# Optimization experiments

Measured on AMD Instinct MI355X. Metric: run time of the kernel, lower is better.

The kernel has to match this reference:

```python
import jax, jax.numpy as jnp
import numpy as np

B, L, H = 4, 1024, 1024
NH, HD = 16, 64
ND = NH * HD
ITERS = 4
U = 5  # MSA1 ring window size (hard-coded in source)


def _conv1x1(w, b, x):  # w [O,C], b [O], x [B,C,L] -> [B,O,L]  (Conv2d 1x1 == per-position linear)
    return jnp.einsum('oc,bcl->bol', w, x) + b[None, :, None]


def _layernorm(x, s, b, eps=1e-5):  # x [B,H,L]; LayerNorm over channel dim H
    mu = x.mean(1, keepdims=True)
    var = ((x - mu) ** 2).mean(1, keepdims=True)
    return (x - mu) / jnp.sqrt(var + eps) * s[None, :, None] + b[None, :, None]


def _msa1(x, ax, wq, bq, wk, bk, wv, bv, wo, bo):
    # x [B,H,L] normalized nodes; ax [B,H,2,L] (ring embedding + relay)
    b, h, l = x.shape
    q = _conv1x1(wq, bq, x).reshape(b, NH, HD, l)
    k = _conv1x1(wk, bk, x).reshape(b, NH, HD, l)
    v = _conv1x1(wv, bv, x).reshape(b, NH, HD, l)
    pad = U // 2
    kp = jnp.pad(k, ((0, 0), (0, 0), (0, 0), (pad, pad)))
    vp = jnp.pad(v, ((0, 0), (0, 0), (0, 0), (pad, pad)))
    # F.unfold with (U,1) kernel along L == stack of U shifted views
    kw = jnp.stack([kp[..., u:u + l] for u in range(U)], axis=3)  # [B,NH,HD,U,L]
    vw = jnp.stack([vp[..., u:u + l] for u in range(U)], axis=3)
    al = ax.shape[2]
    ak = (jnp.einsum('oc,bcal->boal', wk, ax) + bk[None, :, None, None]).reshape(b, NH, HD, al, l)
    av = (jnp.einsum('oc,bcal->boal', wv, ax) + bv[None, :, None, None]).reshape(b, NH, HD, al, l)
    kw = jnp.concatenate([kw, ak], axis=3)  # [B,NH,HD,U+2,L]
    vw = jnp.concatenate([vw, av], axis=3)
    scores = (q[:, :, :, None, :] * kw).sum(2) / np.sqrt(HD)  # [B,NH,U+2,L]
    alphas = jax.nn.softmax(scores, axis=2)
    att = (alphas[:, :, None, :, :] * vw).sum(3).reshape(b, ND, l)
    return _conv1x1(wo, bo, att)  # [B,H,L]


def _msa2(relay, y, smask, wq, bq, wk, bk, wo, bo):
    # relay [B,H]; y [B,H,L+1]; smask [B,L+1] True at padding
    b = relay.shape[0]
    q = (jnp.einsum('oc,bc->bo', wq, relay) + bq).reshape(b, NH, HD)
    k = _conv1x1(wk, bk, y).reshape(b, NH, HD, -1)
    pre = jnp.einsum('bnd,bndl->bnl', q, k) / np.sqrt(HD)
    pre = jnp.where(smask[:, None, :], -1e10, pre)
    alphas = jax.nn.softmax(pre, axis=-1)
    # NOTE: source has v = k (WV output unused) -- reproduced faithfully
    att = jnp.einsum('bnl,bndl->bnd', alphas, k).reshape(b, ND)
    return jnp.einsum('oc,bc->bo', wo, att) + bo  # [B,H]


def _star_forward(data, mask, ln_s, ln_b, rwq, rwq_b, rwk, rwk_b, rwv, rwv_b, rwo, rwo_b,
                  swq, swq_b, swk, swk_b, swo, swo_b):
    b, l, h = data.shape
    pad_mask = (mask == 0)  # True at padding positions
    smask = jnp.concatenate([jnp.zeros((b, 1), bool), pad_mask], axis=1)  # [B,L+1]
    embs = jnp.transpose(data, (0, 2, 1))  # [B,H,L]
    nodes = embs
    relay = embs.mean(2)  # [B,H]
    for i in range(ITERS):
        xn = _layernorm(nodes, ln_s[i], ln_b[i])
        ax = jnp.stack([embs, jnp.broadcast_to(relay[:, :, None], embs.shape)], axis=2)  # [B,H,2,L]
        ring = _msa1(xn, ax, rwq[i], rwq_b[i], rwk[i], rwk_b[i], rwv[i], rwv_b[i], rwo[i], rwo_b[i])
        nodes = nodes + jax.nn.leaky_relu(ring)
        y = jnp.concatenate([relay[:, :, None], nodes], axis=2)  # [B,H,L+1]
        relay = jax.nn.leaky_relu(_msa2(relay, y, smask, swq[i], swq_b[i], swk[i], swk_b[i], swo[i], swo_b[i]))
        nodes = jnp.where(pad_mask[:, None, :], 0.0, nodes)
    return jnp.transpose(nodes, (0, 2, 1)), relay  # [B,L,H], [B,H]


def setup_inputs() -> dict:
    key = jax.random.key(0)
    ks = jax.random.split(key, 16)
    def p(k, shape):
        return jax.random.normal(k, shape, jnp.float32) * 0.02
    return dict(
        data=jax.random.normal(ks[0], (B, L, H), jnp.float32),
        mask=jax.random.randint(ks[1], (B, L), 0, 2).astype(jnp.int32),
        ln_s=jnp.ones((ITERS, H), jnp.float32),
        ln_b=jnp.zeros((ITERS, H), jnp.float32),
        rwq=p(ks[2], (ITERS, ND, H)), rwq_b=p(ks[3], (ITERS, ND)),
        rwk=p(ks[4], (ITERS, ND, H)), rwk_b=p(ks[5], (ITERS, ND)),
        rwv=p(ks[6], (ITERS, ND, H)), rwv_b=p(ks[7], (ITERS, ND)),
        rwo=p(ks[8], (ITERS, H, ND)), rwo_b=p(ks[9], (ITERS, H)),
        swq=p(ks[10], (ITERS, ND, H)), swq_b=p(ks[11], (ITERS, ND)),
        swk=p(ks[12], (ITERS, ND, H)), swk_b=p(ks[13], (ITERS, ND)),
        swo=p(ks[14], (ITERS, H, ND)), swo_b=p(ks[15], (ITERS, H)),
    )


def reference(data, mask, ln_s, ln_b, rwq, rwq_b, rwk, rwk_b, rwv, rwv_b, rwo, rwo_b,
              swq, swq_b, swk, swk_b, swo, swo_b):
    return _star_forward(data, mask, ln_s, ln_b, rwq, rwq_b, rwk, rwk_b, rwv, rwv_b,
                         rwo, rwo_b, swq, swq_b, swk, swk_b, swo, swo_b)
```

## Files before the change

### kernel.cpp

```cpp
#include <hip/hip_runtime.h>
#include <math.h>

namespace {

constexpr int B_ = 4, L_ = 1024, H_ = 1024, NH_ = 16, HD_ = 64, ND_ = 1024, ITERS_ = 4;

typedef unsigned short u16;
typedef __attribute__((ext_vector_type(8))) short short8;
typedef __attribute__((ext_vector_type(4))) float f32x4;

__device__ inline u16 f2bf(float f) {
  unsigned u = __builtin_bit_cast(unsigned, f);
  u += 0x7FFFu + ((u >> 16) & 1u);
  return (u16)(u >> 16);
}
__device__ inline float bf2f(u16 v) {
  unsigned u = ((unsigned)v) << 16;
  return __builtin_bit_cast(float, u);
}

__device__ inline void gl_lds16(const u16* g, u16* l) {
  __builtin_amdgcn_global_load_lds((const __attribute__((address_space(1))) void*)g,
                                   (__attribute__((address_space(3))) void*)l, 16, 0, 0);
}

__global__ void k_prep(const float* __restrict__ data, const float* __restrict__ rwq,
                       const float* __restrict__ rwk, const float* __restrict__ rwv,
                       const float* __restrict__ rwo, const float* __restrict__ swk,
                       u16* __restrict__ embs_bf, u16* __restrict__ wq_bf,
                       u16* __restrict__ wk_bf, u16* __restrict__ wv_bf,
                       u16* __restrict__ wo_bf, u16* __restrict__ swk_bf,
                       float* __restrict__ nodes) {
  int i = blockIdx.x * 256 + threadIdx.x;
  int which = blockIdx.y;
  if (which == 6) {
    reinterpret_cast<float4*>(nodes)[i] = reinterpret_cast<const float4*>(data)[i];
    return;
  }
  const float* src;
  u16* dst;
  switch (which) {
    case 0: src = data; dst = embs_bf; break;
    case 1: src = rwq; dst = wq_bf; break;
    case 2: src = rwk; dst = wk_bf; break;
    case 3: src = rwv; dst = wv_bf; break;
    case 4: src = rwo; dst = wo_bf; break;
    default: src = swk; dst = swk_bf; break;
  }
  float4 v = reinterpret_cast<const float4*>(src)[i];
  ushort4 o;
  o.x = f2bf(v.x); o.y = f2bf(v.y); o.z = f2bf(v.z); o.w = f2bf(v.w);
  reinterpret_cast<ushort4*>(dst)[i] = o;
}

__global__ void k_relay_part(const float* __restrict__ data, float* __restrict__ part) {
  int b = blockIdx.z, chunk = blockIdx.y;
  int c = blockIdx.x * 256 + threadIdx.x;
  const float* p = data + ((size_t)b * L_ + chunk * 128) * H_ + c;
  float acc = 0.f;
  for (int l = 0; l < 128; ++l) acc += p[(size_t)l * H_];
  part[((size_t)b * 8 + chunk) * H_ + c] = acc;
}
__global__ void k_relay_reduce(const float* __restrict__ part, float* __restrict__ relay) {
  int i = blockIdx.x * 256 + threadIdx.x;
  int b = i >> 10, c = i & 1023;
  float acc = 0.f;
  for (int j = 0; j < 8; ++j) acc += part[((size_t)b * 8 + j) * H_ + c];
  relay[i] = acc * (1.f / (float)L_);
}

__global__ __launch_bounds__(256) void k_layernorm_bf(float* __restrict__ nodes,
                                                      const float* __restrict__ s,
                                                      const float* __restrict__ bb,
                                                      const int* __restrict__ mask,
                                                      u16* __restrict__ y, int do_zero) {
  int row = blockIdx.x * 4 + (threadIdx.x >> 6);
  int lane = threadIdx.x & 63;
  int b = row >> 10, l = row & 1023;
  bool pad = do_zero && (mask[b * L_ + l] == 0);
  float4* xr = reinterpret_cast<float4*>(nodes + (size_t)row * H_);
  float4 v[4];
  float sum = 0.f, sq = 0.f;
#pragma unroll
  for (int j = 0; j < 4; ++j) {
    v[j] = pad ? float4{0.f, 0.f, 0.f, 0.f} : xr[lane + 64 * j];
    sum += v[j].x + v[j].y + v[j].z + v[j].w;
    sq += v[j].x * v[j].x + v[j].y * v[j].y + v[j].z * v[j].z + v[j].w * v[j].w;
  }
  if (pad) {
#pragma unroll
    for (int j = 0; j < 4; ++j) xr[lane + 64 * j] = float4{0.f, 0.f, 0.f, 0.f};
  }
#pragma unroll
  for (int off = 32; off; off >>= 1) {
    sum += __shfl_xor(sum, off);
    sq += __shfl_xor(sq, off);
  }
  float mu = sum * (1.f / (float)H_);
  float rstd = rsqrtf(sq * (1.f / (float)H_) - mu * mu + 1e-5f);
  ushort4* yr = reinterpret_cast<ushort4*>(y + (size_t)row * H_);
#pragma unroll
  for (int j = 0; j < 4; ++j) {
    int c4 = lane + 64 * j;
    float4 sc = reinterpret_cast<const float4*>(s)[c4];
    float4 bc = reinterpret_cast<const float4*>(bb)[c4];
    ushort4 o;
    o.x = f2bf((v[j].x - mu) * rstd * sc.x + bc.x);
    o.y = f2bf((v[j].y - mu) * rstd * sc.y + bc.y);
    o.z = f2bf((v[j].z - mu) * rstd * sc.z + bc.z);
    o.w = f2bf((v[j].w - mu) * rstd * sc.w + bc.w);
    yr[c4] = o;
  }
}


#define GEMM_PROLOGUE(XPTR, WPTR)                                              \
  __shared__ __align__(16) u16 sX[128 * 32];                                   \
  __shared__ __align__(16) u16 sW[128 * 32];                                   \
  const int t = threadIdx.x;                                                   \
  const int w = t >> 6, lane = t & 63;                                         \
  const int wm = w >> 1, wn = w & 1;                                           \
  const int r4 = lane >> 2, slot = lane & 3;                                   \
  const int rowS0 = w * 16 + r4, rowS1 = 64 + rowS0;                           \
  const int colS0 = ((slot ^ ((rowS0 >> 1) & 3)) << 3);                        \
  const int colS1 = ((slot ^ ((rowS1 >> 1) & 3)) << 3);                        \
  const u16* gX0 = (XPTR) + (size_t)(bm + rowS0) * 1024 + colS0;               \
  const u16* gX1 = (XPTR) + (size_t)(bm + rowS1) * 1024 + colS1;               \
  const u16* gW0 = (WPTR) + (size_t)(bn + rowS0) * 1024 + colS0;               \
  const u16* gW1 = (WPTR) + (size_t)(bn + rowS1) * 1024 + colS1;               \
  u16* lX0 = sX + (size_t)w * 512;                                             \
  u16* lX1 = sX + (size_t)(4 + w) * 512;                                       \
  u16* lW0 = sW + (size_t)w * 512;                                             \
  u16* lW1 = sW + (size_t)(4 + w) * 512;                                       \
  const int kidx = (((lane >> 4) ^ ((lane >> 1) & 3)) << 3);                   \
  f32x4 acc[4][4];                                                             \
  _Pragma("unroll") for (int i_ = 0; i_ < 4; ++i_)                             \
      _Pragma("unroll") for (int j_ = 0; j_ < 4; ++j_)                         \
          acc[i_][j_] = f32x4{0.f, 0.f, 0.f, 0.f};

#define GEMM_KLOOP(AROWBASE, BROWBASE, ASRC, BSRC)                             \
  for (int ck = 0; ck < 1024; ck += 32) {                                      \
    gl_lds16(gX0, lX0);                                                        \
    gl_lds16(gX1, lX1);                                                        \
    gl_lds16(gW0, lW0);                                                        \
    gl_lds16(gW1, lW1);                                                        \
    gX0 += 32; gX1 += 32; gW0 += 32; gW1 += 32;                                \
    __syncthreads();                                                           \
    short8 af_[4], bf_[4];                                                     \
    _Pragma("unroll") for (int mf = 0; mf < 4; ++mf)                           \
        af_[mf] = *reinterpret_cast<const short8*>(                            \
            &ASRC[((AROWBASE) + mf * 16) * 32 + kidx]);                        \
    _Pragma("unroll") for (int nf = 0; nf < 4; ++nf)                           \
        bf_[nf] = *reinterpret_cast<const short8*>(                            \
            &BSRC[((BROWBASE) + nf * 16) * 32 + kidx]);                        \
    _Pragma("unroll") for (int mf = 0; mf < 4; ++mf)                           \
        _Pragma("unroll") for (int nf = 0; nf < 4; ++nf)                       \
            acc[mf][nf] = __builtin_amdgcn_mfma_f32_16x16x32_bf16(             \
                af_[mf], bf_[nf], acc[mf][nf], 0, 0, 0);                       \
    __syncthreads();                                                          \
  }

__global__ __launch_bounds__(256) void k_gemm5(const u16* __restrict__ wq,
                                               const u16* __restrict__ wk,
                                               const u16* __restrict__ wv,
                                               const float* __restrict__ bq,
                                               const float* __restrict__ bk,
                                               const float* __restrict__ bv,
                                               const u16* __restrict__ xn,
                                               const u16* __restrict__ embs,
                                               u16* __restrict__ Y) {
  const int bm = blockIdx.x * 128;
  const int which = blockIdx.y >> 3;
  const int bn = (blockIdx.y & 7) * 128;
  const u16* W = (which == 0) ? wq : ((which == 1 || which == 3) ? wk : wv);
  const float* bias = (which == 0) ? bq : ((which == 1 || which == 3) ? bk : bv);
  const u16* X = (which < 3) ? xn : embs;
  u16* Yw = Y + (size_t)which * ((size_t)B_ * L_ * ND_);

  GEMM_PROLOGUE(X, W)
  const int rW = wm * 64 + (lane & 15);
  const int rX = wn * 64 + (lane & 15);
  GEMM_KLOOP(rW, rX, sW, sX)

#pragma unroll
  for (int mo = 0; mo < 4; ++mo) {
    int o0 = bn + wm * 64 + mo * 16 + ((lane >> 4) << 2);
    float4 bs = *reinterpret_cast<const float4*>(bias + o0);
#pragma unroll
    for (int nl = 0; nl < 4; ++nl) {
      int bl = bm + wn * 64 + nl * 16 + (lane & 15);
      f32x4 vv = acc[mo][nl];
      ushort4 ov;
      ov.x = f2bf(vv[0] + bs.x);
      ov.y = f2bf(vv[1] + bs.y);
      ov.z = f2bf(vv[2] + bs.z);
      ov.w = f2bf(vv[3] + bs.w);
      *reinterpret_cast<ushort4*>(&Yw[(size_t)bl * 1024 + o0]) = ov;
    }
  }
}

__global__ __launch_bounds__(256) void k_gemm_wo(const u16* __restrict__ W,
                                                 const float* __restrict__ bias,
                                                 const u16* __restrict__ X,
                                                 float* __restrict__ nodes,
                                                 u16* __restrict__ nodes_bf) {
  const int bm = blockIdx.x * 128;
  const int bn = blockIdx.y * 128;
  GEMM_PROLOGUE(X, W)
  const int rW = wm * 64 + (lane & 15);
  const int rX = wn * 64 + (lane & 15);
  GEMM_KLOOP(rW, rX, sW, sX)

#pragma unroll
  for (int mo = 0; mo < 4; ++mo) {
    int o0 = bn + wm * 64 + mo * 16 + ((lane >> 4) << 2);
    float4 bs = *reinterpret_cast<const float4*>(bias + o0);
#pragma unroll
    for (int nl = 0; nl < 4; ++nl) {
      int bl = bm + wn * 64 + nl * 16 + (lane & 15);
      size_t ni = (size_t)bl * 1024 + o0;
      float4 cur = *reinterpret_cast<const float4*>(&nodes[ni]);
      f32x4 vv = acc[mo][nl];
      float r0 = vv[0] + bs.x; r0 = cur.x + (r0 > 0.f ? r0 : 0.01f * r0);
      float r1 = vv[1] + bs.y; r1 = cur.y + (r1 > 0.f ? r1 : 0.01f * r1);
      float r2 = vv[2] + bs.z; r2 = cur.z + (r2 > 0.f ? r2 : 0.01f * r2);
      float r3 = vv[3] + bs.w; r3 = cur.w + (r3 > 0.f ? r3 : 0.01f * r3);
      *reinterpret_cast<float4*>(&nodes[ni]) = float4{r0, r1, r2, r3};
      ushort4 ov;
      ov.x = f2bf(r0); ov.y = f2bf(r1); ov.z = f2bf(r2); ov.w = f2bf(r3);
      *reinterpret_cast<ushort4*>(&nodes_bf[ni]) = ov;
    }
  }
}

__global__ __launch_bounds__(256) void k_gemm_kkb(const u16* __restrict__ W,
                                                  const float* __restrict__ bias,
                                                  const u16* __restrict__ X,
                                                  float* __restrict__ Y) {
  const int bm = blockIdx.x * 128;
  const int bn = blockIdx.y * 128;
  GEMM_PROLOGUE(X, W)
  const int rX = wm * 64 + (lane & 15);
  const int rW = wn * 64 + (lane & 15);
  GEMM_KLOOP(rX, rW, sX, sW)

#pragma unroll
  for (int nf = 0; nf < 4; ++nf) {
    int o = bn + wn * 64 + nf * 16 + (lane & 15);
    float bs = bias[o];
#pragma unroll
    for (int mf = 0; mf < 4; ++mf) {
      int gl = bm + wm * 64 + mf * 16 + ((lane >> 4) << 2);
      int b = gl >> 10, l = gl & 1023;
      size_t yi = ((size_t)(b * 1024 + o)) * (size_t)(L_ + 1) + 1 + l;
      f32x4 v = acc[mf][nf];
#pragma unroll
      for (int r = 0; r < 4; ++r) Y[yi + r] = v[r] + bs;
    }
  }
}

__global__ __launch_bounds__(256) void k_matvec2(const float* __restrict__ W0,
                                                 const float* __restrict__ b0,
                                                 float* __restrict__ y0, long sB0, long sO0,
                                                 const float* __restrict__ W1,
                                                 const float* __restrict__ b1,
                                                 float* __restrict__ y1, long sB1, long sO1,
                                                 const float* __restrict__ x) {
  int b = blockIdx.y;
  int z = blockIdx.z;
  const float* W = z ? W1 : W0;
  const float* bias = z ? b1 : b0;
  float* y = z ? y1 : y0;
  long sB = z ? sB1 : sB0, sO = z ? sO1 : sO0;
  int o = blockIdx.x * 4 + (threadIdx.x >> 6);
  int lane = threadIdx.x & 63;
  const float* wr = W + (size_t)o * 1024;
  const float* xb = x + (size_t)b * 1024;
  float acc = 0.f;
  for (int c = lane; c < 1024; c += 64) acc += wr[c] * xb[c];
#pragma unroll
  for (int off = 32; off; off >>= 1) acc += __shfl_xor(acc, off);
  if (lane == 0) y[(size_t)b * sB + (size_t)o * sO] = acc + bias[o];
}

__global__ __launch_bounds__(256) void k_matvec(const float* __restrict__ W,
                                                const float* __restrict__ bias,
                                                const float* __restrict__ x,
                                                float* __restrict__ y) {
  int b = blockIdx.y;
  int o = blockIdx.x * 4 + (threadIdx.x >> 6);
  int lane = threadIdx.x & 63;
  const float* wr = W + (size_t)o * 1024;
  const float* xb = x + (size_t)b * 1024;
  float acc = 0.f;
  for (int c = lane; c < 1024; c += 64) acc += wr[c] * xb[c];
#pragma unroll
  for (int off = 32; off; off >>= 1) acc += __shfl_xor(acc, off);
  if (lane == 0) {
    acc += bias[o];
    y[(size_t)b * 1024 + o] = acc > 0.f ? acc : 0.01f * acc;
  }
}

__global__ __launch_bounds__(256) void k_msa1(const u16* __restrict__ q,
                                              const u16* __restrict__ k,
                                              const u16* __restrict__ v,
                                              const u16* __restrict__ ke,
                                              const u16* __restrict__ ve,
                                              const float* __restrict__ rk,
                                              const float* __restrict__ rv,
                                              u16* __restrict__ attbf) {
  int t = threadIdx.x;
  int head = t & 15, dh = (t >> 4) & 1, lsub = t >> 5;
  int l = blockIdx.x * 8 + lsub;
  int b = blockIdx.z;
  size_t row = ((size_t)(b * 1024 + l)) * 1024 + head * 64 + dh * 32;
  size_t rbase = (size_t)b * 1024 + head * 64 + dh * 32;

  float qf[32];
  {
    const short8* qp = reinterpret_cast<const short8*>(q + row);
#pragma unroll
    for (int j = 0; j < 4; ++j) {
      short8 qv = qp[j];
#pragma unroll
      for (int e = 0; e < 8; ++e) qf[j * 8 + e] = bf2f((u16)qv[e]);
    }
  }
  float s[7];
#pragma unroll
  for (int u = 0; u < 5; ++u) {
    int lk = l + u - 2;
    float su = 0.f;
    if (lk >= 0 && lk < L_) {
      const short8* kp =
          reinterpret_cast<const short8*>(k + ((size_t)(b * 1024 + lk)) * 1024 + head * 64 + dh * 32);
#pragma unroll
      for (int j = 0; j < 4; ++j) {
        short8 kv = kp[j];
#pragma unroll
        for (int e = 0; e < 8; ++e) su = fmaf(qf[j * 8 + e], bf2f((u16)kv[e]), su);
      }
    }
    s[u] = su;
  }
  {
    float su = 0.f;
    const short8* kp = reinterpret_cast<const short8*>(ke + row);
#pragma unroll
    for (int j = 0; j < 4; ++j) {
      short8 kv = kp[j];
#pragma unroll
      for (int e = 0; e < 8; ++e) su = fmaf(qf[j * 8 + e], bf2f((u16)kv[e]), su);
    }
    s[5] = su;
  }
  {
    float su = 0.f;
    const float4* rp = reinterpret_cast<const float4*>(rk + rbase);
#pragma unroll
    for (int j = 0; j < 8; ++j) {
      float4 r4 = rp[j];
      su = fmaf(qf[j * 4 + 0], r4.x, su);
      su = fmaf(qf[j * 4 + 1], r4.y, su);
      su = fmaf(qf[j * 4 + 2], r4.z, su);
      su = fmaf(qf[j * 4 + 3], r4.w, su);
    }
    s[6] = su;
  }
#pragma unroll
  for (int u = 0; u < 7; ++u) s[u] += __shfl_xor(s[u], 16);
  float m = -1e30f;
#pragma unroll
  for (int u = 0; u < 7; ++u) {
    s[u] *= 0.125f;
    m = fmaxf(m, s[u]);
  }
  float e[7], tot = 0.f;
#pragma unroll
  for (int u = 0; u < 7; ++u) {
    e[u] = expf(s[u] - m);
    tot += e[u];
  }
  float inv = 1.f / tot;
#pragma unroll
  for (int u = 0; u < 7; ++u) e[u] *= inv;

  float av[32];
  {
    const float4* rp = reinterpret_cast<const float4*>(rv + rbase);
#pragma unroll
    for (int j = 0; j < 8; ++j) {
      float4 r4 = rp[j];
      av[j * 4 + 0] = e[6] * r4.x;
      av[j * 4 + 1] = e[6] * r4.y;
      av[j * 4 + 2] = e[6] * r4.z;
      av[j * 4 + 3] = e[6] * r4.w;
    }
  }
  {
    const short8* vp = reinterpret_cast<const short8*>(ve + row);
#pragma unroll
    for (int j = 0; j < 4; ++j) {
      short8 vv = vp[j];
#pragma unroll
      for (int ee = 0; ee < 8; ++ee) av[j * 8 + ee] = fmaf(e[5], bf2f((u16)vv[ee]), av[j * 8 + ee]);
    }
  }
#pragma unroll
  for (int u = 0; u < 5; ++u) {
    int lk = l + u - 2;
    if (lk >= 0 && lk < L_) {
      const short8* vp =
          reinterpret_cast<const short8*>(v + ((size_t)(b * 1024 + lk)) * 1024 + head * 64 + dh * 32);
#pragma unroll
      for (int j = 0; j < 4; ++j) {
        short8 vv = vp[j];
#pragma unroll
        for (int ee = 0; ee < 8; ++ee) av[j * 8 + ee] = fmaf(e[u], bf2f((u16)vv[ee]), av[j * 8 + ee]);
      }
    }
  }
  u16 ob[32];
#pragma unroll
  for (int j = 0; j < 32; ++j) ob[j] = f2bf(av[j]);
  uint4* d4 = reinterpret_cast<uint4*>(attbf + row);
  const uint4* s4 = reinterpret_cast<const uint4*>(ob);
#pragma unroll
  for (int j = 0; j < 4; ++j) d4[j] = s4[j];
}

__global__ __launch_bounds__(1024) void k_msa2(const float* __restrict__ rq,
                                               const float* __restrict__ kk,
                                               const int* __restrict__ mask,
                                               float* __restrict__ satt) {
  int n = blockIdx.x, b = blockIdx.y;
  int t = threadIdx.x;
  __shared__ float sq_[HD_];
  __shared__ float se[L_ + 1];
  __shared__ float swsum[16];
  __shared__ float stot;
  size_t rb = (size_t)(b * NH_ + n) * HD_;
  if (t < HD_) sq_[t] = rq[rb + t];
  __syncthreads();
  const float* kb = kk + rb * (size_t)(L_ + 1);
  float ls = 0.f;
  for (int p = t; p < L_ + 1; p += 1024) {
    float e;
    if (p > 0 && mask[b * L_ + p - 1] == 0) {
      e = 0.f;
    } else {
      float acc = 0.f;
      for (int d = 0; d < HD_; ++d) acc = fmaf(sq_[d], kb[(size_t)d * (L_ + 1) + p], acc);
      e = expf(acc * 0.125f);
    }
    se[p] = e;
    ls += e;
  }
  int lane = t & 63, w = t >> 6;
#pragma unroll
  for (int off = 32; off; off >>= 1) ls += __shfl_xor(ls, off);
  if (lane == 0) swsum[w] = ls;
  __syncthreads();
  if (t == 0) {
    float tot = 0.f;
    for (int j = 0; j < 16; ++j) tot += swsum[j];
    stot = 1.f / tot;
  }
  __syncthreads();
  float inv = stot;
  float acc[4] = {0.f, 0.f, 0.f, 0.f};
  const float* kw = kb + (size_t)(w * 4) * (L_ + 1);
  for (int p = lane; p < L_ + 1; p += 64) {
    float e = se[p];
#pragma unroll
    for (int j = 0; j < 4; ++j) acc[j] = fmaf(e, kw[(size_t)j * (L_ + 1) + p], acc[j]);
  }
#pragma unroll
  for (int j = 0; j < 4; ++j) {
    float a = acc[j];
#pragma unroll
    for (int off = 32; off; off >>= 1) a += __shfl_xor(a, off);
    if (lane == 0) satt[rb + w * 4 + j] = a * inv;
  }
}

__global__ void k_final(const float* __restrict__ nodes, const int* __restrict__ mask,
                        float* __restrict__ out) {
  int i = blockIdx.x * 256 + threadIdx.x;
  int row = i >> 8;
  int b = row >> 10, l = row & 1023;
  float4 v = (mask[b * L_ + l] == 0) ? float4{0.f, 0.f, 0.f, 0.f}
                                     : reinterpret_cast<const float4*>(nodes)[i];
  reinterpret_cast<float4*>(out)[i] = v;
}

__global__ void k_copy_relay(const float* __restrict__ relay, float* __restrict__ out) {
  int i = blockIdx.x * 256 + threadIdx.x;
  out[i] = relay[i];
}

}

extern "C" void kernel_launch(void* const* d_in, const int* in_sizes, int n_in,
                              void* d_out, int out_size, void* d_ws, size_t ws_size,
                              hipStream_t stream) {
  (void)in_sizes; (void)n_in; (void)out_size; (void)ws_size;
  const float* data = (const float*)d_in[0];
  const int* mask = (const int*)d_in[1];
  const float* ln_s = (const float*)d_in[2];
  const float* ln_b = (const float*)d_in[3];
  const float* rwq = (const float*)d_in[4];
  const float* rwq_b = (const float*)d_in[5];
  const float* rwk = (const float*)d_in[6];
  const float* rwk_b = (const float*)d_in[7];
  const float* rwv = (const float*)d_in[8];
  const float* rwv_b = (const float*)d_in[9];
  const float* rwo = (const float*)d_in[10];
  const float* rwo_b = (const float*)d_in[11];
  const float* swq = (const float*)d_in[12];
  const float* swq_b = (const float*)d_in[13];
  const float* swk = (const float*)d_in[14];
  const float* swk_b = (const float*)d_in[15];
  const float* swo = (const float*)d_in[16];
  const float* swo_b = (const float*)d_in[17];
  float* out = (float*)d_out;

  const size_t SZ = (size_t)B_ * ND_ * L_;
  float* f = (float*)d_ws;
  float* nodes = f; f += SZ;
  float* kkb = f; f += (size_t)B_ * ND_ * (L_ + 1);
  float* part = f; f += (size_t)B_ * 8 * H_;
  float* relay = f; f += B_ * H_;
  float* rk = f; f += B_ * ND_;
  float* rv = f; f += B_ * ND_;
  float* rq = f; f += B_ * ND_;
  float* satt = f; f += B_ * ND_;
  u16* u = (u16*)f;
  u16* xn_bf = u; u += SZ;
  u16* embs_bf = u; u += SZ;
  u16* att_bf = u; u += SZ;
  u16* nodes_bf = u; u += SZ;
  u16* qkv5_bf = u; u += 5 * SZ;
  u16* wq_bf = u; u += SZ;
  u16* wk_bf = u; u += SZ;
  u16* wv_bf = u; u += SZ;
  u16* wo_bf = u; u += SZ;
  u16* swk_bf = u; u += SZ;

  k_prep<<<dim3(4096, 7), 256, 0, stream>>>(data, rwq, rwk, rwv, rwo, swk,
                                            embs_bf, wq_bf, wk_bf, wv_bf, wo_bf, swk_bf, nodes);
  k_relay_part<<<dim3(H_ / 256, 8, B_), 256, 0, stream>>>(data, part);
  k_relay_reduce<<<dim3((B_ * H_) / 256), 256, 0, stream>>>(part, relay);

  for (int i = 0; i < ITERS_; ++i) {
    const u16* wq_i = wq_bf + (size_t)i * ND_ * H_;
    const u16* wk_i = wk_bf + (size_t)i * ND_ * H_;
    const u16* wv_i = wv_bf + (size_t)i * ND_ * H_;
    const u16* wo_i = wo_bf + (size_t)i * H_ * ND_;
    const u16* sk_i = swk_bf + (size_t)i * ND_ * H_;

    k_layernorm_bf<<<dim3(B_ * L_ / 4), 256, 0, stream>>>(nodes, ln_s + i * H_, ln_b + i * H_,
                                                          mask, xn_bf, i > 0 ? 1 : 0);
    k_gemm5<<<dim3(32, 40), 256, 0, stream>>>(wq_i, wk_i, wv_i,
                                              rwq_b + i * ND_, rwk_b + i * ND_, rwv_b + i * ND_,
                                              xn_bf, embs_bf, qkv5_bf);
    k_matvec2<<<dim3(256, B_, 2), 256, 0, stream>>>(
        rwk + (size_t)i * ND_ * H_, rwk_b + i * ND_, rk, ND_, 1,
        rwv + (size_t)i * ND_ * H_, rwv_b + i * ND_, rv, ND_, 1, relay);
    k_msa1<<<dim3(L_ / 8, 1, B_), 256, 0, stream>>>(qkv5_bf, qkv5_bf + SZ, qkv5_bf + 2 * SZ,
                                                    qkv5_bf + 3 * SZ, qkv5_bf + 4 * SZ, rk, rv, att_bf);
    k_gemm_wo<<<dim3(32, 8), 256, 0, stream>>>(wo_i, rwo_b + i * H_, att_bf, nodes, nodes_bf);
    k_matvec2<<<dim3(256, B_, 2), 256, 0, stream>>>(
        swq + (size_t)i * ND_ * H_, swq_b + i * ND_, rq, ND_, 1,
        swk + (size_t)i * ND_ * H_, swk_b + i * ND_, kkb, (long)ND_ * (L_ + 1), L_ + 1, relay);
    k_gemm_kkb<<<dim3(32, 8), 256, 0, stream>>>(sk_i, swk_b + i * ND_, nodes_bf, kkb);
    k_msa2<<<dim3(NH_, B_), 1024, 0, stream>>>(rq, kkb, mask, satt);
    k_matvec<<<dim3(256, B_), 256, 0, stream>>>(swo + (size_t)i * H_ * ND_, swo_b + i * H_, satt, relay);
  }
  k_final<<<4096, 256, 0, stream>>>(nodes, mask, out);
  k_copy_relay<<<dim3((B_ * H_) / 256), 256, 0, stream>>>(relay, out + (size_t)B_ * L_ * H_);
}
```

Baseline: 767.8 us.

## Double-buffer GEMM LDS tiles and split MSA2 across sequence chunks

```diff
diff --git a/kernel.cpp b/kernel.cpp
--- a/kernel.cpp
+++ b/kernel.cpp
@@ -115,8 +115,8 @@
 
 
 #define GEMM_PROLOGUE(XPTR, WPTR)                                              \
-  __shared__ __align__(16) u16 sX[128 * 32];                                   \
-  __shared__ __align__(16) u16 sW[128 * 32];                                   \
+  __shared__ __align__(16) u16 sX[2][128 * 32];                                \
+  __shared__ __align__(16) u16 sW[2][128 * 32];                                \
   const int t = threadIdx.x;                                                   \
   const int w = t >> 6, lane = t & 63;                                         \
   const int wm = w >> 1, wn = w & 1;                                           \
@@ -128,36 +128,45 @@
   const u16* gX1 = (XPTR) + (size_t)(bm + rowS1) * 1024 + colS1;               \
   const u16* gW0 = (WPTR) + (size_t)(bn + rowS0) * 1024 + colS0;               \
   const u16* gW1 = (WPTR) + (size_t)(bn + rowS1) * 1024 + colS1;               \
-  u16* lX0 = sX + (size_t)w * 512;                                             \
-  u16* lX1 = sX + (size_t)(4 + w) * 512;                                       \
-  u16* lW0 = sW + (size_t)w * 512;                                             \
-  u16* lW1 = sW + (size_t)(4 + w) * 512;                                       \
   const int kidx = (((lane >> 4) ^ ((lane >> 1) & 3)) << 3);                   \
   f32x4 acc[4][4];                                                             \
   _Pragma("unroll") for (int i_ = 0; i_ < 4; ++i_)                             \
       _Pragma("unroll") for (int j_ = 0; j_ < 4; ++j_)                         \
           acc[i_][j_] = f32x4{0.f, 0.f, 0.f, 0.f};
 
-#define GEMM_KLOOP(AROWBASE, BROWBASE, ASRC, BSRC)                             \
+#define GEMM_STAGE(BUF)                                                        \
+  gl_lds16(gX0, sX[BUF] + w * 512);                                            \
+  gl_lds16(gX1, sX[BUF] + (4 + w) * 512);                                      \
+  gl_lds16(gW0, sW[BUF] + w * 512);                                            \
+  gl_lds16(gW1, sW[BUF] + (4 + w) * 512);                                      \
+  gX0 += 32; gX1 += 32; gW0 += 32; gW1 += 32;
+
+#define GEMM_KLOOP_DB(AROWBASE, BROWBASE, ASRC, BSRC)                          \
+  int cur = 0;                                                                 \
+  GEMM_STAGE(0)                                                                \
   for (int ck = 0; ck < 1024; ck += 32) {                                      \
-    gl_lds16(gX0, lX0);                                                        \
-    gl_lds16(gX1, lX1);                                                        \
-    gl_lds16(gW0, lW0);                                                        \
-    gl_lds16(gW1, lW1);                                                        \
-    gX0 += 32; gX1 += 32; gW0 += 32; gW1 += 32;                                \
-    __syncthreads();                                                           \
+    if (ck < 992) {                                                            \
+      GEMM_STAGE(cur ^ 1)                                                      \
+      asm volatile("s_waitcnt vmcnt(4)" ::: "memory");                         \
+    } else {                                                                   \
+      asm volatile("s_waitcnt vmcnt(0)" ::: "memory");                         \
+    }                                                                          \
+    __builtin_amdgcn_s_barrier();                                              \
+    __builtin_amdgcn_sched_barrier(0);                                         \
     short8 af_[4], bf_[4];                                                     \
     _Pragma("unroll") for (int mf = 0; mf < 4; ++mf)                           \
         af_[mf] = *reinterpret_cast<const short8*>(                            \
-            &ASRC[((AROWBASE) + mf * 16) * 32 + kidx]);                        \
+            &ASRC[cur][((AROWBASE) + mf * 16) * 32 + kidx]);                   \
     _Pragma("unroll") for (int nf = 0; nf < 4; ++nf)                           \
         bf_[nf] = *reinterpret_cast<const short8*>(                            \
-            &BSRC[((BROWBASE) + nf * 16) * 32 + kidx]);                        \
+            &BSRC[cur][((BROWBASE) + nf * 16) * 32 + kidx]);                   \
     _Pragma("unroll") for (int mf = 0; mf < 4; ++mf)                           \
         _Pragma("unroll") for (int nf = 0; nf < 4; ++nf)                       \
             acc[mf][nf] = __builtin_amdgcn_mfma_f32_16x16x32_bf16(             \
                 af_[mf], bf_[nf], acc[mf][nf], 0, 0, 0);                       \
-    __syncthreads();                                                          \
+    __builtin_amdgcn_sched_barrier(0);                                         \
+    __builtin_amdgcn_s_barrier();                                              \
+    cur ^= 1;                                                                  \
   }
 
 __global__ __launch_bounds__(256) void k_gemm5(const u16* __restrict__ wq,
@@ -180,7 +189,7 @@
   GEMM_PROLOGUE(X, W)
   const int rW = wm * 64 + (lane & 15);
   const int rX = wn * 64 + (lane & 15);
-  GEMM_KLOOP(rW, rX, sW, sX)
+  GEMM_KLOOP_DB(rW, rX, sW, sX)
 
 #pragma unroll
   for (int mo = 0; mo < 4; ++mo) {
@@ -210,7 +219,7 @@
   GEMM_PROLOGUE(X, W)
   const int rW = wm * 64 + (lane & 15);
   const int rX = wn * 64 + (lane & 15);
-  GEMM_KLOOP(rW, rX, sW, sX)
+  GEMM_KLOOP_DB(rW, rX, sW, sX)
 
 #pragma unroll
   for (int mo = 0; mo < 4; ++mo) {
@@ -220,12 +229,12 @@
     for (int nl = 0; nl < 4; ++nl) {
       int bl = bm + wn * 64 + nl * 16 + (lane & 15);
       size_t ni = (size_t)bl * 1024 + o0;
-      float4 cur = *reinterpret_cast<const float4*>(&nodes[ni]);
+      float4 curv = *reinterpret_cast<const float4*>(&nodes[ni]);
       f32x4 vv = acc[mo][nl];
-      float r0 = vv[0] + bs.x; r0 = cur.x + (r0 > 0.f ? r0 : 0.01f * r0);
-      float r1 = vv[1] + bs.y; r1 = cur.y + (r1 > 0.f ? r1 : 0.01f * r1);
-      float r2 = vv[2] + bs.z; r2 = cur.z + (r2 > 0.f ? r2 : 0.01f * r2);
-      float r3 = vv[3] + bs.w; r3 = cur.w + (r3 > 0.f ? r3 : 0.01f * r3);
+      float r0 = vv[0] + bs.x; r0 = curv.x + (r0 > 0.f ? r0 : 0.01f * r0);
+      float r1 = vv[1] + bs.y; r1 = curv.y + (r1 > 0.f ? r1 : 0.01f * r1);
+      float r2 = vv[2] + bs.z; r2 = curv.z + (r2 > 0.f ? r2 : 0.01f * r2);
+      float r3 = vv[3] + bs.w; r3 = curv.w + (r3 > 0.f ? r3 : 0.01f * r3);
       *reinterpret_cast<float4*>(&nodes[ni]) = float4{r0, r1, r2, r3};
       ushort4 ov;
       ov.x = f2bf(r0); ov.y = f2bf(r1); ov.z = f2bf(r2); ov.w = f2bf(r3);
@@ -243,7 +252,7 @@
   GEMM_PROLOGUE(X, W)
   const int rX = wm * 64 + (lane & 15);
   const int rW = wn * 64 + (lane & 15);
-  GEMM_KLOOP(rX, rW, sX, sW)
+  GEMM_KLOOP_DB(rX, rW, sX, sW)
 
 #pragma unroll
   for (int nf = 0; nf < 4; ++nf) {
@@ -432,22 +441,22 @@
   for (int j = 0; j < 4; ++j) d4[j] = s4[j];
 }
 
-__global__ __launch_bounds__(1024) void k_msa2(const float* __restrict__ rq,
+__global__ __launch_bounds__(256) void k_msa2p(const float* __restrict__ rq,
                                                const float* __restrict__ kk,
                                                const int* __restrict__ mask,
-                                               float* __restrict__ satt) {
-  int n = blockIdx.x, b = blockIdx.y;
-  int t = threadIdx.x;
+                                               float* __restrict__ pw,
+                                               float* __restrict__ pE) {
+  int n = blockIdx.x, c = blockIdx.y, b = blockIdx.z;
+  int tid = threadIdx.x;
   __shared__ float sq_[HD_];
-  __shared__ float se[L_ + 1];
-  __shared__ float swsum[16];
-  __shared__ float stot;
+  __shared__ float se[260];
   size_t rb = (size_t)(b * NH_ + n) * HD_;
-  if (t < HD_) sq_[t] = rq[rb + t];
+  if (tid < HD_) sq_[tid] = rq[rb + tid];
   __syncthreads();
   const float* kb = kk + rb * (size_t)(L_ + 1);
-  float ls = 0.f;
-  for (int p = t; p < L_ + 1; p += 1024) {
+  int p0 = c * 256;
+  {
+    int p = p0 + tid;
     float e;
     if (p > 0 && mask[b * L_ + p - 1] == 0) {
       e = 0.f;
@@ -456,35 +465,51 @@
       for (int d = 0; d < HD_; ++d) acc = fmaf(sq_[d], kb[(size_t)d * (L_ + 1) + p], acc);
       e = expf(acc * 0.125f);
     }
-    se[p] = e;
-    ls += e;
-  }
-  int lane = t & 63, w = t >> 6;
-#pragma unroll
-  for (int off = 32; off; off >>= 1) ls += __shfl_xor(ls, off);
-  if (lane == 0) swsum[w] = ls;
+    se[tid] = e;
+  }
+  int nP = 256;
+  if (c == 3) {
+    nP = 257;
+    if (tid == 0) {
+      float e;
+      if (mask[b * L_ + 1023] == 0) {
+        e = 0.f;
+      } else {
+        float acc = 0.f;
+        for (int d = 0; d < HD_; ++d) acc = fmaf(sq_[d], kb[(size_t)d * (L_ + 1) + 1024], acc);
+        e = expf(acc * 0.125f);
+      }
+      se[256] = e;
+    }
+  }
   __syncthreads();
-  if (t == 0) {
-    float tot = 0.f;
-    for (int j = 0; j < 16; ++j) tot += swsum[j];
-    stot = 1.f / tot;
-  }
-  __syncthreads();
-  float inv = stot;
-  float acc[4] = {0.f, 0.f, 0.f, 0.f};
-  const float* kw = kb + (size_t)(w * 4) * (L_ + 1);
-  for (int p = lane; p < L_ + 1; p += 64) {
-    float e = se[p];
-#pragma unroll
-    for (int j = 0; j < 4; ++j) acc[j] = fmaf(e, kw[(size_t)j * (L_ + 1) + p], acc[j]);
-  }
-#pragma unroll
-  for (int j = 0; j < 4; ++j) {
-    float a = acc[j];
+  int lane = tid & 63, w = tid >> 6;
+  if (w == 0) {
+    float E = 0.f;
+    for (int i = lane; i < nP; i += 64) E += se[i];
+#pragma unroll
+    for (int off = 32; off; off >>= 1) E += __shfl_xor(E, off);
+    if (lane == 0) pE[((size_t)(b * NH_ + n)) * 4 + c] = E;
+  }
+  for (int dd = 0; dd < 16; ++dd) {
+    int d = w * 16 + dd;
+    const float* kd = kb + (size_t)d * (L_ + 1) + p0;
+    float a = 0.f;
+    for (int i = lane; i < nP; i += 64) a = fmaf(se[i], kd[i], a);
 #pragma unroll
     for (int off = 32; off; off >>= 1) a += __shfl_xor(a, off);
-    if (lane == 0) satt[rb + w * 4 + j] = a * inv;
-  }
+    if (lane == 0) pw[(((size_t)(b * NH_ + n)) * 4 + c) * HD_ + d] = a;
+  }
+}
+
+__global__ void k_msa2r(const float* __restrict__ pw, const float* __restrict__ pE,
+                        float* __restrict__ satt) {
+  int i = blockIdx.x * 256 + threadIdx.x;
+  int bn = i >> 6, d = i & 63;
+  float E = pE[bn * 4 + 0] + pE[bn * 4 + 1] + pE[bn * 4 + 2] + pE[bn * 4 + 3];
+  float ws = pw[((size_t)bn * 4 + 0) * HD_ + d] + pw[((size_t)bn * 4 + 1) * HD_ + d] +
+             pw[((size_t)bn * 4 + 2) * HD_ + d] + pw[((size_t)bn * 4 + 3) * HD_ + d];
+  satt[i] = ws / E;
 }
 
 __global__ void k_final(const float* __restrict__ nodes, const int* __restrict__ mask,
@@ -538,6 +563,8 @@
   float* rv = f; f += B_ * ND_;
   float* rq = f; f += B_ * ND_;
   float* satt = f; f += B_ * ND_;
+  float* pw = f; f += (size_t)B_ * NH_ * 4 * HD_;
+  float* pE = f; f += B_ * NH_ * 4;
   u16* u = (u16*)f;
   u16* xn_bf = u; u += SZ;
   u16* embs_bf = u; u += SZ;
@@ -577,7 +604,8 @@
         swq + (size_t)i * ND_ * H_, swq_b + i * ND_, rq, ND_, 1,
         swk + (size_t)i * ND_ * H_, swk_b + i * ND_, kkb, (long)ND_ * (L_ + 1), L_ + 1, relay);
     k_gemm_kkb<<<dim3(32, 8), 256, 0, stream>>>(sk_i, swk_b + i * ND_, nodes_bf, kkb);
-    k_msa2<<<dim3(NH_, B_), 1024, 0, stream>>>(rq, kkb, mask, satt);
+    k_msa2p<<<dim3(NH_, 4, B_), 256, 0, stream>>>(rq, kkb, mask, pw, pE);
+    k_msa2r<<<dim3((B_ * NH_ * HD_) / 256), 256, 0, stream>>>(pw, pE, satt);
     k_matvec<<<dim3(256, B_), 256, 0, stream>>>(swo + (size_t)i * H_ * ND_, swo_b + i * H_, satt, relay);
   }
   k_final<<<4096, 256, 0, stream>>>(nodes, mask, out);
```

Measured after the change: 764.2 us. Within noise of the previous version (-0.5%).
